# Performance work log

Measured on AMD Instinct MI355X. Metric: run time of the kernel, lower is better.

Reference implementation:

```python
import jax
import jax.numpy as jnp
from jax import lax
import numpy as np

B, ND, H, W = 8, 8, 512, 512
CONF = 0.9
MARGIN = 3.0
MIN_CLUSTER = 50
MAX_X = 102.4
MPP0, MPP1 = 0.2, 0.2
K = 32  # max clusters (torch version grows an unbounded python list)


def setup_inputs() -> dict:
    key = jax.random.key(0)
    k1, k2, k3, k4, k5, k6 = jax.random.split(key, 6)
    return {
        "seg": jax.random.uniform(k1, (B, 1, H, W), dtype=jnp.float32),
        "embedding": jax.random.normal(k2, (B, ND, H, W), dtype=jnp.float32),
        "offset_pred": jax.random.normal(k3, (B, 1, H, W), dtype=jnp.float32),
        "z_pred": jax.random.normal(k4, (B, 1, H, W), dtype=jnp.float32),
        "intrinsic": jax.random.normal(k5, (B, 3, 3), dtype=jnp.float32),
        "extrinsic": jax.random.normal(k6, (B, 4, 4), dtype=jnp.float32),
    }


def _cluster_one(seg_flat, emb_flat):
    # seg_flat: [N], emb_flat: [N, ND]. Greedy sequential embedding clustering
    # (naive_cluster_nd): running-mean centers, assign to nearest center if
    # within MARGIN else open a new one. Fixed K slots; counts>0 marks active.
    nd = emb_flat.shape[1]

    def step(carry, xs):
        centers, counts = carry  # [K, nd], [K]
        s, e = xs
        valid = s >= CONF
        d = jnp.sqrt(jnp.sum((centers - e) ** 2, axis=1))
        d = jnp.where(counts > 0, d, jnp.inf)
        cid_min = jnp.argmin(d).astype(jnp.int32)
        join = d[cid_min] < MARGIN
        n_active = jnp.sum(counts > 0).astype(jnp.int32)
        cid = jnp.where(join, cid_min, jnp.minimum(n_active, K - 1))
        cnt = counts[cid]
        new_c = jnp.where(join, (centers[cid] * cnt + e) / (cnt + 1.0), e)
        centers = jnp.where(valid, centers.at[cid].set(new_c), centers)
        counts = jnp.where(valid, counts.at[cid].add(1.0), counts)
        return (centers, counts), jnp.where(valid, cid, -1)

    init = (jnp.zeros((K, nd), emb_flat.dtype), jnp.zeros((K,), emb_flat.dtype))
    (_, _), cids = lax.scan(step, init, (seg_flat, emb_flat))
    return cids  # [N] int32, -1 = background


def reference(seg, embedding, offset_pred, z_pred, intrinsic, extrinsic):
    b, nd, h, w = embedding.shape
    seg_flat = seg[:, 0].reshape(b, h * w)
    emb_flat = embedding.reshape(b, nd, h * w).transpose(0, 2, 1)  # [B, N, nd]
    cids = jax.vmap(_cluster_one)(seg_flat, emb_flat).reshape(b, h, w)
    lanes = jnp.where(cids >= 0, cids + 1, 0)  # [B, H, W], 0 = background

    # mean_col_by_row_with_offset_z: per (batch, lane, row) mean of col+offset and z
    offset_y = jax.nn.sigmoid(offset_pred[:, 0])          # [B, H, W]
    x_adj = jnp.arange(w, dtype=seg.dtype)[None, None, :] + offset_y
    zc = z_pred[:, 0]
    b_idx = jnp.arange(b)[:, None, None]
    h_idx = jnp.arange(h)[None, :, None]
    seg_ids = ((b_idx * (K + 1) + lanes) * h + h_idx).reshape(-1)
    num = b * (K + 1) * h

    def ssum(v):
        return jax.ops.segment_sum(v.reshape(-1), seg_ids, num_segments=num).reshape(b, K + 1, h)[:, 1:]

    cnt = ssum(jnp.ones((b, h, w), seg.dtype))            # [B, K, H]
    mean_x = ssum(x_adj) / jnp.maximum(cnt, 1.0)
    mean_z = ssum(zc) / jnp.maximum(cnt, 1.0)

    size = cnt.sum(-1)                                    # cluster pixel count
    n_rows = (cnt > 0).sum(-1)                            # rows per lane
    valid = (cnt > 0) & (size[:, :, None] >= MIN_CLUSTER) & (n_rows[:, :, None] >= 2)

    # ego-coordinate transform from forward()
    x_world = (MAX_X / MPP0 - (jnp.arange(h, dtype=seg.dtype) + 0.5)) * MPP0  # [H]
    x_world = jnp.broadcast_to(x_world, (b, K, h))
    y_world = -(mean_x - (w // 2)) * MPP1
    points = jnp.stack([x_world, y_world, mean_z], axis=1)  # [B, 3, K, H]
    points = jnp.where(valid[:, None], points, 0.0)
    return points, valid
```

## Files before the change

kernel.cpp:

```cpp
#include <hip/hip_runtime.h>

#define HW_ (512 * 512)
#define B_ 8
#define H_ 512
#define W_ 512
#define K_ 32
#define CH_ 16
#define CHPIX_ (HW_ / CH_)

__global__ void k_count(const float* __restrict__ seg, int* __restrict__ chunkCnt) {
  const int blk = blockIdx.x;
  const int t = threadIdx.x;
  const float4* __restrict__ s4 = (const float4*)(seg + (size_t)blk * CHPIX_) + (size_t)t * 16;
  int cnt = 0;
#pragma unroll
  for (int j = 0; j < 16; ++j) {
    float4 v = s4[j];
    cnt += (v.x >= 0.9f) + (v.y >= 0.9f) + (v.z >= 0.9f) + (v.w >= 0.9f);
  }
  __shared__ int red[256];
  red[t] = cnt;
  __syncthreads();
  for (int off = 128; off > 0; off >>= 1) {
    if (t < off) red[t] += red[t + off];
    __syncthreads();
  }
  if (t == 0) chunkCnt[blk] = red[0];
}

__global__ void k_scan(const int* __restrict__ chunkCnt, int* __restrict__ chunkBase,
                       int* __restrict__ nvalid, int cap) {
  const int t = threadIdx.x;
  if (t < B_ * CH_) {
    const int b = t / CH_, c = t % CH_;
    int base = 0;
    for (int q = 0; q < c; ++q) base += chunkCnt[b * CH_ + q];
    chunkBase[t] = base;
    if (c == CH_ - 1) nvalid[b] = min(base + chunkCnt[t], cap);
  }
}

__global__ void k_fill(const float* __restrict__ seg, const float* __restrict__ emb,
                       const int* __restrict__ chunkBase, unsigned char* __restrict__ lanes,
                       int* __restrict__ idxC, float* __restrict__ embC, int cap) {
  const int blk = blockIdx.x;
  const int b = blk / CH_;
  const int t = threadIdx.x;
  const size_t pixbase = (size_t)blk * CHPIX_ + (size_t)t * 64;
  const float4* __restrict__ s4 = (const float4*)(seg + pixbase);

  int cnt = 0;
#pragma unroll
  for (int j = 0; j < 16; ++j) {
    float4 v = s4[j];
    cnt += (v.x >= 0.9f) + (v.y >= 0.9f) + (v.z >= 0.9f) + (v.w >= 0.9f);
  }
  __shared__ int pre[256];
  pre[t] = cnt;
  __syncthreads();
  for (int off = 1; off < 256; off <<= 1) {
    int mine = pre[t];
    int add = (t >= off) ? pre[t - off] : 0;
    __syncthreads();
    pre[t] = mine + add;
    __syncthreads();
  }
  int w = chunkBase[blk] + pre[t] - cnt;

  uint4 z = {0u, 0u, 0u, 0u};
  uint4* lz = (uint4*)(lanes + pixbase);
  lz[0] = z; lz[1] = z; lz[2] = z; lz[3] = z;

  const float* __restrict__ eb = emb + (size_t)b * 8 * HW_;
  const int pixInB = (int)(pixbase - (size_t)b * HW_);
  for (int j = 0; j < 16; ++j) {
    float4 v = s4[j];
    float sv[4] = {v.x, v.y, v.z, v.w};
#pragma unroll
    for (int q = 0; q < 4; ++q) {
      if (sv[q] >= 0.9f && w < cap) {
        const int p = pixInB + j * 4 + q;
        idxC[(size_t)b * cap + w] = p;
        float* dst = embC + ((size_t)b * cap + w) * 8;
#pragma unroll
        for (int dd = 0; dd < 8; ++dd) dst[dd] = eb[(size_t)dd * HW_ + p];
        ++w;
      }
    }
  }
}


#define TILE_ 32

__device__ __forceinline__ void stage16(const float* g, float* l) {
  __builtin_amdgcn_global_load_lds(
      (const __attribute__((address_space(1))) void*)g,
      (__attribute__((address_space(3))) void*)l, 16, 0, 0);
}

#define RLF(V, L) __uint_as_float((unsigned)__builtin_amdgcn_readlane(__float_as_int(V), (L)))

#define STEPP(J)                                                                     \
  do {                                                                               \
    const float e0 = RLF(td.x, 2 * (J)), e1 = RLF(td.y, 2 * (J));                    \
    const float e2 = RLF(td.z, 2 * (J)), e3 = RLF(td.w, 2 * (J));                    \
    const float e4 = RLF(td.x, 2 * (J) + 1), e5 = RLF(td.y, 2 * (J) + 1);            \
    const float e6 = RLF(td.z, 2 * (J) + 1), e7 = RLF(td.w, 2 * (J) + 1);            \
    float t0 = C0 - e0, t1 = C1 - e1, t2 = C2 - e2, t3 = C3 - e3;                    \
    float t4 = C4 - e4, t5 = C5 - e5, t6 = C6 - e6, t7 = C7 - e7;                    \
    float a0 = t0 * t0 + t1 * t1;                                                    \
    float a1 = t2 * t2 + t3 * t3;                                                    \
    float a2 = t4 * t4 + t5 * t5;                                                    \
    float a3 = t6 * t6 + t7 * t7;                                                    \
    float dsq = (a0 + a1) + (a2 + a3);                                               \
    unsigned db = __float_as_uint(dsq);                                              \
    unsigned dbm = db > emptyBits ? db : emptyBits;         \
    unsigned key = (dbm & 0xFFFFFFE0u) | (unsigned)cl;             \
    unsigned mn = key, mr;                                                           \
    mr = (unsigned)__builtin_amdgcn_update_dpp(0, (int)mn, 0xB1, 0xF, 0xF, true);    \
    mn = mn < mr ? mn : mr;                                                          \
    mr = (unsigned)__builtin_amdgcn_update_dpp(0, (int)mn, 0x4E, 0xF, 0xF, true);    \
    mn = mn < mr ? mn : mr;                                                          \
    mr = (unsigned)__builtin_amdgcn_update_dpp(0, (int)mn, 0x141, 0xF, 0xF, true);   \
    mn = mn < mr ? mn : mr;                                                          \
    mr = (unsigned)__builtin_amdgcn_update_dpp(0, (int)mn, 0x140, 0xF, 0xF, true);   \
    mn = mn < mr ? mn : mr;                                                          \
    unsigned q0 = (unsigned)__builtin_amdgcn_readlane((int)mn, 0);                   \
    unsigned q1 = (unsigned)__builtin_amdgcn_readlane((int)mn, 16);                  \
    unsigned mv = q0 < q1 ? q0 : q1;                            \
    bool join = mv < 0x41100000u;            \
    int cid = join ? (int)(mv & 31u) : (nact < 31 ? nact : 31);                      \
    nact += join ? 0 : 1;                                                            \
    bool own = (cl == cid);                                                          \
    float wj = join ? inv : 1.0f;                                                    \
    float w = own ? wj : 0.0f;                                                       \
    C0 = __builtin_fmaf(t0, -w, C0);                                                 \
    C1 = __builtin_fmaf(t1, -w, C1);                                                 \
    C2 = __builtin_fmaf(t2, -w, C2);                                                 \
    C3 = __builtin_fmaf(t3, -w, C3);                                                 \
    C4 = __builtin_fmaf(t4, -w, C4);                                                 \
    C5 = __builtin_fmaf(t5, -w, C5);                                                 \
    C6 = __builtin_fmaf(t6, -w, C6);                                                 \
    C7 = __builtin_fmaf(t7, -w, C7);                                                 \
    cnt += own ? 1.0f : 0.0f;                                                        \
    inv = __builtin_amdgcn_rcpf(cnt + 1.0f);          \
    emptyBits = own ? 0u : emptyBits;                                                \
    pk |= (unsigned long long)(unsigned)(cid + 1) << (((J) & 7) * 8);                \
    if (((J) & 7) == 7) {                                                            \
      if (lane == 0) *(unsigned long long*)(cptr + ((J) & ~7)) = pk;                 \
      pk = 0ULL;                                                                     \
    }                                                                                \
  } while (0)

__global__ __launch_bounds__(64, 1) void k_cluster(const float* __restrict__ embC,
                                                   const int* __restrict__ nvalid,
                                                   unsigned char* __restrict__ cidArr,
                                                   int cap) {
  __shared__ float lds[512];
  const int b = blockIdx.x;
  const int lane = threadIdx.x;
  const int cl = lane & 31;
  const int n = nvalid[b];
  if (n <= 0) return;
  const int nTiles = (n + TILE_ - 1) / TILE_;

  const float* src = embC + (size_t)b * cap * 8 + lane * 4;
  unsigned char* cidB = cidArr + (size_t)b * HW_;

  float C0 = 0.f, C1 = 0.f, C2 = 0.f, C3 = 0.f, C4 = 0.f, C5 = 0.f, C6 = 0.f, C7 = 0.f;
  float cnt = 0.f, inv = 1.0f;
  unsigned emptyBits = 0x7F800000u;
  int nact = 0;
  unsigned long long pk = 0ULL;

  stage16(src, lds);
  asm volatile("s_waitcnt vmcnt(0)" ::: "memory");
  __builtin_amdgcn_sched_barrier(0);
  float4 td = ((const float4*)lds)[lane];

  for (int ti = 0; ti < nTiles; ++ti) {
    unsigned char* cptr = cidB + ti * TILE_;
    if (ti + 1 < nTiles)
      stage16(src + (size_t)(ti + 1) * 256, lds + ((ti + 1) & 1) * 128);

    STEPP(0);  STEPP(1);  STEPP(2);  STEPP(3);
    STEPP(4);  STEPP(5);  STEPP(6);  STEPP(7);
    STEPP(8);  STEPP(9);  STEPP(10); STEPP(11);
    STEPP(12); STEPP(13); STEPP(14); STEPP(15);
    STEPP(16); STEPP(17); STEPP(18); STEPP(19);
    STEPP(20); STEPP(21); STEPP(22); STEPP(23);
    STEPP(24); STEPP(25); STEPP(26); STEPP(27);
    STEPP(28); STEPP(29); STEPP(30); STEPP(31);

    if (ti + 1 < nTiles) {
      asm volatile("s_waitcnt vmcnt(4)" ::: "memory");
      __builtin_amdgcn_sched_barrier(0);
      td = ((const float4*)(lds + ((ti + 1) & 1) * 128))[lane];
    }
  }
}

__global__ void k_scatter(const unsigned char* __restrict__ cidArr,
                          const int* __restrict__ idxC, const int* __restrict__ nvalid,
                          unsigned char* __restrict__ lanes, int cap) {
  const int b = blockIdx.y;
  const int n = nvalid[b];
  for (int j = blockIdx.x * blockDim.x + threadIdx.x; j < n; j += gridDim.x * blockDim.x) {
    lanes[(size_t)b * HW_ + idxC[(size_t)b * cap + j]] = cidArr[(size_t)b * HW_ + j];
  }
}

__global__ void k_rowsum(const unsigned char* __restrict__ lanes,
                         const float* __restrict__ offp, const float* __restrict__ zp,
                         float* __restrict__ cnt, float* __restrict__ sx,
                         float* __restrict__ sz) {
  const int bh = blockIdx.x;
  const int b = bh >> 9, h = bh & 511;
  __shared__ float sc[33], sxx[33], szz[33];
  const int t = threadIdx.x;
  if (t < 33) { sc[t] = 0.f; sxx[t] = 0.f; szz[t] = 0.f; }
  __syncthreads();
  const size_t base = (size_t)bh * W_;
  for (int x = t; x < W_; x += 256) {
    int ln = lanes[base + x];
    float o = offp[base + x];
    float sig = 1.0f / (1.0f + expf(-o));
    float xa = (float)x + sig;
    float zv = zp[base + x];
    atomicAdd(&sc[ln], 1.0f);
    atomicAdd(&sxx[ln], xa);
    atomicAdd(&szz[ln], zv);
  }
  __syncthreads();
  if (t >= 1 && t < 33) {
    size_t o = ((size_t)b * K_ + (t - 1)) * H_ + h;
    cnt[o] = sc[t]; sx[o] = sxx[t]; sz[o] = szz[t];
  }
}

__global__ void k_final(const float* __restrict__ cnt, const float* __restrict__ sx,
                        const float* __restrict__ sz, float* __restrict__ out) {
  const int bk = blockIdx.x;
  const int b = bk >> 5, k = bk & 31;
  const int h = threadIdx.x;
  const size_t o = (size_t)bk * H_ + h;
  float c = cnt[o];
  float sc_ = c, sn = (c > 0.f) ? 1.f : 0.f;
#pragma unroll
  for (int off = 32; off >= 1; off >>= 1) {
    sc_ += __shfl_down(sc_, off);
    sn += __shfl_down(sn, off);
  }
  __shared__ float rs[8], rn[8], tot[2];
  const int wid = h >> 6, lid = h & 63;
  if (lid == 0) { rs[wid] = sc_; rn[wid] = sn; }
  __syncthreads();
  if (h == 0) {
    float a = 0, bb = 0;
#pragma unroll
    for (int q = 0; q < 8; ++q) { a += rs[q]; bb += rn[q]; }
    tot[0] = a; tot[1] = bb;
  }
  __syncthreads();
  float size = tot[0], nrows = tot[1];
  bool valid = (c > 0.f) && (size >= 50.f) && (nrows >= 2.f);
  float mx = sx[o] / fmaxf(c, 1.f);
  float mz = sz[o] / fmaxf(c, 1.f);
  float xw = (512.0f - ((float)h + 0.5f)) * 0.2f;
  float yw = -(mx - 256.0f) * 0.2f;
  out[((size_t)(b * 3 + 0) * K_ + k) * H_ + h] = valid ? xw : 0.f;
  out[((size_t)(b * 3 + 1) * K_ + k) * H_ + h] = valid ? yw : 0.f;
  out[((size_t)(b * 3 + 2) * K_ + k) * H_ + h] = valid ? mz : 0.f;
  out[(size_t)B_ * 3 * K_ * H_ + (size_t)bk * H_ + h] = valid ? 1.f : 0.f;
}

extern "C" void kernel_launch(void* const* d_in, const int* in_sizes, int n_in,
                              void* d_out, int out_size, void* d_ws, size_t ws_size,
                              hipStream_t stream) {
  const float* seg  = (const float*)d_in[0];
  const float* emb  = (const float*)d_in[1];
  const float* offp = (const float*)d_in[2];
  const float* zp   = (const float*)d_in[3];
  float* out = (float*)d_out;
  char* ws = (char*)d_ws;

  const size_t lanesOff = 0;
  const size_t cntOff   = (size_t)B_ * HW_;
  const size_t sxOff    = cntOff + (size_t)B_ * K_ * H_ * 4;
  const size_t szOff    = sxOff  + (size_t)B_ * K_ * H_ * 4;
  const size_t nvOff    = szOff  + (size_t)B_ * K_ * H_ * 4;
  const size_t ccOff    = nvOff + 256;
  const size_t cbOff    = ccOff + 1024;
  const size_t cidOff   = cbOff + 1024;
  const size_t idxOff   = cidOff + (size_t)B_ * HW_;
  size_t avail = (ws_size > idxOff + 4096) ? (ws_size - idxOff - 4096) : 0;
  long long capLL = (long long)(avail / ((size_t)B_ * 36));
  if (capLL > (long long)HW_) capLL = HW_;
  if (capLL < 1) capLL = 1;
  const int cap = (int)capLL;
  const size_t embOff = idxOff + (size_t)B_ * cap * 4;

  unsigned char* lanes = (unsigned char*)(ws + lanesOff);
  float* cnt = (float*)(ws + cntOff);
  float* sx  = (float*)(ws + sxOff);
  float* sz  = (float*)(ws + szOff);
  int* nvalid = (int*)(ws + nvOff);
  int* chunkCnt  = (int*)(ws + ccOff);
  int* chunkBase = (int*)(ws + cbOff);
  unsigned char* cidArr = (unsigned char*)(ws + cidOff);
  int* idxC   = (int*)(ws + idxOff);
  float* embC = (float*)(ws + embOff);

  k_count<<<B_ * CH_, 256, 0, stream>>>(seg, chunkCnt);
  k_scan<<<1, 128, 0, stream>>>(chunkCnt, chunkBase, nvalid, cap);
  k_fill<<<B_ * CH_, 256, 0, stream>>>(seg, emb, chunkBase, lanes, idxC, embC, cap);
  k_cluster<<<B_, 64, 0, stream>>>(embC, nvalid, cidArr, cap);
  k_scatter<<<dim3(64, B_), 256, 0, stream>>>(cidArr, idxC, nvalid, lanes, cap);
  k_rowsum<<<B_ * H_, 256, 0, stream>>>(lanes, offp, zp, cnt, sx, sz);
  k_final<<<B_ * K_, H_, 0, stream>>>(cnt, sx, sz, out);
}
```

Baseline: 3.119 ms.

## Restructure cluster step with incremental distance update and packed FMA

Rewrites the sequential greedy clustering inner step so each pixel's squared distance is derived from the previous distance via an algebraic update (dsq' = w²·dsq − 2w·g + spec), which shortens the serial dependency chain per step. It also uses packed float2 FMAs, an inline-asm DPP min reduction, 64-pixel tiles with double-buffered LDS prefetch, and one wide store of the cluster ids per tile. In exchange it adds floating-point reassociation that can change near-threshold join decisions, and it reads one element past the tile boundary, which requires the workspace capacity to be even and padded.

Measured after the change: 3.883 ms. 24.5% more time.

```diff
diff --git a/kernel.cpp b/kernel.cpp
--- a/kernel.cpp
+++ b/kernel.cpp
@@ -7,6 +7,8 @@
 #define K_ 32
 #define CH_ 16
 #define CHPIX_ (HW_ / CH_)
+
+typedef float float2v __attribute__((ext_vector_type(2)));
 
 __global__ void k_count(const float* __restrict__ seg, int* __restrict__ chunkCnt) {
   const int blk = blockIdx.x;
@@ -91,7 +93,7 @@
 }
 
 
-#define TILE_ 32
+#define TILE_ 64
 
 __device__ __forceinline__ void stage16(const float* g, float* l) {
   __builtin_amdgcn_global_load_lds(
@@ -100,64 +102,72 @@
 }
 
 #define RLF(V, L) __uint_as_float((unsigned)__builtin_amdgcn_readlane(__float_as_int(V), (L)))
-
-#define STEPP(J)                                                                     \
-  do {                                                                               \
-    const float e0 = RLF(td.x, 2 * (J)), e1 = RLF(td.y, 2 * (J));                    \
-    const float e2 = RLF(td.z, 2 * (J)), e3 = RLF(td.w, 2 * (J));                    \
-    const float e4 = RLF(td.x, 2 * (J) + 1), e5 = RLF(td.y, 2 * (J) + 1);            \
-    const float e6 = RLF(td.z, 2 * (J) + 1), e7 = RLF(td.w, 2 * (J) + 1);            \
-    float t0 = C0 - e0, t1 = C1 - e1, t2 = C2 - e2, t3 = C3 - e3;                    \
-    float t4 = C4 - e4, t5 = C5 - e5, t6 = C6 - e6, t7 = C7 - e7;                    \
-    float a0 = t0 * t0 + t1 * t1;                                                    \
-    float a1 = t2 * t2 + t3 * t3;                                                    \
-    float a2 = t4 * t4 + t5 * t5;                                                    \
-    float a3 = t6 * t6 + t7 * t7;                                                    \
-    float dsq = (a0 + a1) + (a2 + a3);                                               \
-    unsigned db = __float_as_uint(dsq);                                              \
-    unsigned dbm = db > emptyBits ? db : emptyBits;         \
-    unsigned key = (dbm & 0xFFFFFFE0u) | (unsigned)cl;             \
-    unsigned mn = key, mr;                                                           \
-    mr = (unsigned)__builtin_amdgcn_update_dpp(0, (int)mn, 0xB1, 0xF, 0xF, true);    \
-    mn = mn < mr ? mn : mr;                                                          \
-    mr = (unsigned)__builtin_amdgcn_update_dpp(0, (int)mn, 0x4E, 0xF, 0xF, true);    \
-    mn = mn < mr ? mn : mr;                                                          \
-    mr = (unsigned)__builtin_amdgcn_update_dpp(0, (int)mn, 0x141, 0xF, 0xF, true);   \
-    mn = mn < mr ? mn : mr;                                                          \
-    mr = (unsigned)__builtin_amdgcn_update_dpp(0, (int)mn, 0x140, 0xF, 0xF, true);   \
-    mn = mn < mr ? mn : mr;                                                          \
-    unsigned q0 = (unsigned)__builtin_amdgcn_readlane((int)mn, 0);                   \
-    unsigned q1 = (unsigned)__builtin_amdgcn_readlane((int)mn, 16);                  \
-    unsigned mv = q0 < q1 ? q0 : q1;                            \
-    bool join = mv < 0x41100000u;            \
-    int cid = join ? (int)(mv & 31u) : (nact < 31 ? nact : 31);                      \
-    nact += join ? 0 : 1;                                                            \
-    bool own = (cl == cid);                                                          \
-    float wj = join ? inv : 1.0f;                                                    \
-    float w = own ? wj : 0.0f;                                                       \
-    C0 = __builtin_fmaf(t0, -w, C0);                                                 \
-    C1 = __builtin_fmaf(t1, -w, C1);                                                 \
-    C2 = __builtin_fmaf(t2, -w, C2);                                                 \
-    C3 = __builtin_fmaf(t3, -w, C3);                                                 \
-    C4 = __builtin_fmaf(t4, -w, C4);                                                 \
-    C5 = __builtin_fmaf(t5, -w, C5);                                                 \
-    C6 = __builtin_fmaf(t6, -w, C6);                                                 \
-    C7 = __builtin_fmaf(t7, -w, C7);                                                 \
-    cnt += own ? 1.0f : 0.0f;                                                        \
-    inv = __builtin_amdgcn_rcpf(cnt + 1.0f);          \
-    emptyBits = own ? 0u : emptyBits;                                                \
-    pk |= (unsigned long long)(unsigned)(cid + 1) << (((J) & 7) * 8);                \
-    if (((J) & 7) == 7) {                                                            \
-      if (lane == 0) *(unsigned long long*)(cptr + ((J) & ~7)) = pk;                 \
-      pk = 0ULL;                                                                     \
-    }                                                                                \
+#define RLU(V, L) ((unsigned)__builtin_amdgcn_readlane((int)(V), (L)))
+#define PKF(A, B, C) __builtin_elementwise_fma((A), (B), (C))
+
+#define STEPX(PK, SH, TD, L)                                                     \
+  do {                                                                           \
+                                        \
+    float dsq = __builtin_fmaf(wp2.x, __builtin_fmaf(wp2.x, dsqq, m2g), dspec);  \
+    unsigned db = __float_as_uint(dsq);                                          \
+    unsigned dbm = db > emptyBits ? db : emptyBits;     \
+    unsigned mn = (dbm & 0xFFFFFFE0u) | (unsigned)cl;                            \
+    asm volatile(                                                                \
+        "s_nop 1\n\t"                                                            \
+        "v_min_u32_dpp %0, %0, %0 quad_perm:[1,0,3,2] row_mask:0xf bank_mask:0xf\n\t" \
+        "s_nop 1\n\t"                                                            \
+        "v_min_u32_dpp %0, %0, %0 quad_perm:[2,3,0,1] row_mask:0xf bank_mask:0xf\n\t" \
+        "s_nop 1\n\t"                                                            \
+        "v_min_u32_dpp %0, %0, %0 row_half_mirror row_mask:0xf bank_mask:0xf\n\t" \
+        "s_nop 1\n\t"                                                            \
+        "v_min_u32_dpp %0, %0, %0 row_mirror row_mask:0xf bank_mask:0xf\n\t"     \
+        "s_nop 1"                                                                \
+        : "+v"(mn));                                                             \
+    unsigned q0 = RLU(mn, 0), q1 = RLU(mn, 16);                                  \
+    unsigned mv = q0 < q1 ? q0 : q1;                        \
+    bool join = mv < 0x41100000u;               \
+    int cid = join ? (int)(mv & 31u) : (nact < 31 ? nact : 31);                  \
+    nact += join ? 0 : 1;                                                        \
+    bool own = (cl == cid);                                                      \
+    float wj = join ? inv : 1.0f;                                                \
+    float w = own ? wj : 0.0f;                                                   \
+                     \
+    C01 = PKF(wp2, t01, C01); C23 = PKF(wp2, t23, C23);                          \
+    C45 = PKF(wp2, t45, C45); C67 = PKF(wp2, t67, C67);                          \
+    t01 = PKF(-wp2, t01, s01); t23 = PKF(-wp2, t23, s23);                        \
+    t45 = PKF(-wp2, t45, s45); t67 = PKF(-wp2, t67, s67);                        \
+                              \
+    float2v e01, e23, e45, e67;                                                  \
+    e01.x = RLF((TD).x, (L)); e01.y = RLF((TD).y, (L));                          \
+    e23.x = RLF((TD).z, (L)); e23.y = RLF((TD).w, (L));                          \
+    e45.x = RLF((TD).x, (L) + 1); e45.y = RLF((TD).y, (L) + 1);                  \
+    e67.x = RLF((TD).z, (L) + 1); e67.y = RLF((TD).w, (L) + 1);                  \
+    s01 = e01 - C01; s23 = e23 - C23; s45 = e45 - C45; s67 = e67 - C67;          \
+    float2v p = s01 * s01;                                                       \
+    p = PKF(s23, s23, p);                                                        \
+    float2v p2 = s45 * s45;                                                      \
+    p2 = PKF(s67, s67, p2);                                                      \
+    p = p + p2;                                                                  \
+    dspec = p.x + p.y;                                                           \
+    float2v gv = t01 * s01;                                                      \
+    gv = PKF(t23, s23, gv);                                                      \
+    float2v gv2 = t45 * s45;                                                     \
+    gv2 = PKF(t67, s67, gv2);                                                    \
+    gv = gv + gv2;                                                               \
+    m2g = -2.0f * (gv.x + gv.y);                                                 \
+    dsqq = dsq;                                                                  \
+    wp2.x = w; wp2.y = w;                                                        \
+    cnt += own ? 1.0f : 0.0f;                                                    \
+    inv = __builtin_amdgcn_rcpf(cnt + 1.0f);                 \
+    emptyBits = own ? 0u : emptyBits;                                            \
+    PK |= (unsigned long long)(unsigned)(cid + 1) << ((SH) * 8);                 \
   } while (0)
 
 __global__ __launch_bounds__(64, 1) void k_cluster(const float* __restrict__ embC,
                                                    const int* __restrict__ nvalid,
                                                    unsigned char* __restrict__ cidArr,
                                                    int cap) {
-  __shared__ float lds[512];
+  __shared__ float lds[1024];
   const int b = blockIdx.x;
   const int lane = threadIdx.x;
   const int cl = lane & 31;
@@ -167,38 +177,85 @@
 
   const float* src = embC + (size_t)b * cap * 8 + lane * 4;
   unsigned char* cidB = cidArr + (size_t)b * HW_;
-
-  float C0 = 0.f, C1 = 0.f, C2 = 0.f, C3 = 0.f, C4 = 0.f, C5 = 0.f, C6 = 0.f, C7 = 0.f;
-  float cnt = 0.f, inv = 1.0f;
+  const float4* f4 = (const float4*)lds;
+
+  float2v C01 = {0.f, 0.f}, C23 = C01, C45 = C01, C67 = C01;
+  float2v t01 = C01, t23 = C01, t45 = C01, t67 = C01;
+  float2v s01, s23, s45, s67;
+  float2v wp2 = {0.f, 0.f};
+  float cnt = 0.f, inv = 1.0f, m2g = 0.f, dsqq = 0.f, dspec;
   unsigned emptyBits = 0x7F800000u;
   int nact = 0;
-  unsigned long long pk = 0ULL;
+  unsigned long long pk0 = 0, pk1 = 0, pk2 = 0, pk3 = 0, pk4 = 0, pk5 = 0, pk6 = 0, pk7 = 0;
 
   stage16(src, lds);
+  stage16(src + 256, lds + 256);
   asm volatile("s_waitcnt vmcnt(0)" ::: "memory");
   __builtin_amdgcn_sched_barrier(0);
-  float4 td = ((const float4*)lds)[lane];
+  float4 td = f4[lane], td2 = f4[64 + lane];
+  float4 tdN = td, td2N = td2;
+
+  s01.x = RLF(td.x, 0); s01.y = RLF(td.y, 0);
+  s23.x = RLF(td.z, 0); s23.y = RLF(td.w, 0);
+  s45.x = RLF(td.x, 1); s45.y = RLF(td.y, 1);
+  s67.x = RLF(td.z, 1); s67.y = RLF(td.w, 1);
+  {
+    float2v p = s01 * s01;
+    p = PKF(s23, s23, p);
+    float2v p2 = s45 * s45;
+    p2 = PKF(s67, s67, p2);
+    p = p + p2;
+    dspec = p.x + p.y;
+  }
+
+#define ROW8(PK, TDa, La, TDb, Lb, TDc, Lc, TDd, Ld, TDe, Le, TDf, Lf, TDg, Lg, TDh, Lh) \
+  STEPX(PK, 0, TDa, La); STEPX(PK, 1, TDb, Lb); STEPX(PK, 2, TDc, Lc); STEPX(PK, 3, TDd, Ld); \
+  STEPX(PK, 4, TDe, Le); STEPX(PK, 5, TDf, Lf); STEPX(PK, 6, TDg, Lg); STEPX(PK, 7, TDh, Lh);
 
   for (int ti = 0; ti < nTiles; ++ti) {
-    unsigned char* cptr = cidB + ti * TILE_;
-    if (ti + 1 < nTiles)
-      stage16(src + (size_t)(ti + 1) * 256, lds + ((ti + 1) & 1) * 128);
-
-    STEPP(0);  STEPP(1);  STEPP(2);  STEPP(3);
-    STEPP(4);  STEPP(5);  STEPP(6);  STEPP(7);
-    STEPP(8);  STEPP(9);  STEPP(10); STEPP(11);
-    STEPP(12); STEPP(13); STEPP(14); STEPP(15);
-    STEPP(16); STEPP(17); STEPP(18); STEPP(19);
-    STEPP(20); STEPP(21); STEPP(22); STEPP(23);
-    STEPP(24); STEPP(25); STEPP(26); STEPP(27);
-    STEPP(28); STEPP(29); STEPP(30); STEPP(31);
-
-    if (ti + 1 < nTiles) {
-      asm volatile("s_waitcnt vmcnt(4)" ::: "memory");
+    const bool more = (ti + 1 < nTiles);
+    if (more) {
+      stage16(src + (size_t)(ti + 1) * 512, lds + ((ti + 1) & 1) * 512);
+      stage16(src + (size_t)(ti + 1) * 512 + 256, lds + ((ti + 1) & 1) * 512 + 256);
+    }
+    ROW8(pk0, td, 2, td, 4, td, 6, td, 8, td, 10, td, 12, td, 14, td, 16)
+    ROW8(pk1, td, 18, td, 20, td, 22, td, 24, td, 26, td, 28, td, 30, td, 32)
+    ROW8(pk2, td, 34, td, 36, td, 38, td, 40, td, 42, td, 44, td, 46, td, 48)
+    ROW8(pk3, td, 50, td, 52, td, 54, td, 56, td, 58, td, 60, td, 62, td2, 0)
+    ROW8(pk4, td2, 2, td2, 4, td2, 6, td2, 8, td2, 10, td2, 12, td2, 14, td2, 16)
+    ROW8(pk5, td2, 18, td2, 20, td2, 22, td2, 24, td2, 26, td2, 28, td2, 30, td2, 32)
+
+    if (more) {
+      asm volatile("s_waitcnt vmcnt(0)" ::: "memory");
       __builtin_amdgcn_sched_barrier(0);
-      td = ((const float4*)(lds + ((ti + 1) & 1) * 128))[lane];
+      const int ph = ((ti + 1) & 1) * 128;
+      tdN = f4[ph + lane];
+      td2N = f4[ph + 64 + lane];
     }
-  }
+    ROW8(pk6, td2, 34, td2, 36, td2, 38, td2, 40, td2, 42, td2, 44, td2, 46, td2, 48)
+    ROW8(pk7, td2, 50, td2, 52, td2, 54, td2, 56, td2, 58, td2, 60, td2, 62, tdN, 0)
+
+    if (lane == 0) {
+      unsigned char* cptr = cidB + ti * TILE_;
+      uint4 v;
+      v.x = (unsigned)pk0; v.y = (unsigned)(pk0 >> 32);
+      v.z = (unsigned)pk1; v.w = (unsigned)(pk1 >> 32);
+      *(uint4*)(cptr + 0) = v;
+      v.x = (unsigned)pk2; v.y = (unsigned)(pk2 >> 32);
+      v.z = (unsigned)pk3; v.w = (unsigned)(pk3 >> 32);
+      *(uint4*)(cptr + 16) = v;
+      v.x = (unsigned)pk4; v.y = (unsigned)(pk4 >> 32);
+      v.z = (unsigned)pk5; v.w = (unsigned)(pk5 >> 32);
+      *(uint4*)(cptr + 32) = v;
+      v.x = (unsigned)pk6; v.y = (unsigned)(pk6 >> 32);
+      v.z = (unsigned)pk7; v.w = (unsigned)(pk7 >> 32);
+      *(uint4*)(cptr + 48) = v;
+    }
+    pk0 = pk1 = pk2 = pk3 = pk4 = pk5 = pk6 = pk7 = 0ULL;
+    td = tdN;
+    td2 = td2N;
+  }
+#undef ROW8
 }
 
 __global__ void k_scatter(const unsigned char* __restrict__ cidArr,
@@ -294,10 +351,11 @@
   const size_t cbOff    = ccOff + 1024;
   const size_t cidOff   = cbOff + 1024;
   const size_t idxOff   = cidOff + (size_t)B_ * HW_;
-  size_t avail = (ws_size > idxOff + 4096) ? (ws_size - idxOff - 4096) : 0;
+  size_t avail = (ws_size > idxOff + 16384) ? (ws_size - idxOff - 16384) : 0;
   long long capLL = (long long)(avail / ((size_t)B_ * 36));
   if (capLL > (long long)HW_) capLL = HW_;
-  if (capLL < 1) capLL = 1;
+  if (capLL < 2) capLL = 2;
+  capLL &= ~1LL;
   const int cap = (int)capLL;
   const size_t embOff = idxOff + (size_t)B_ * cap * 4;
 
```
